# Optimization experiments

Measured on AMD Instinct MI355X. Metric: run time of the kernel, lower is better.

## Reference

```python
import jax, jax.numpy as jnp
import numpy as np

ALPHA = 0.2          # LeakyReLU negative slope
NEG_INF = -9e15      # mask fill value used by the original module


def setup_inputs() -> dict:
    key = jax.random.key(0)
    k1, k2, k3, k4 = jax.random.split(key, 4)
    N, F_in, F_out = 8192, 256, 64
    h = jax.random.normal(k1, (N, F_in), dtype=jnp.float32)
    adj = jax.random.randint(k2, (N, N), 0, 2).astype(jnp.int32)
    # xavier_uniform with gain=1.414
    gain = 1.414
    bW = gain * np.sqrt(6.0 / (F_in + F_out))
    W = jax.random.uniform(k3, (F_in, F_out), dtype=jnp.float32, minval=-bW, maxval=bW)
    ba = gain * np.sqrt(6.0 / (2 * F_out + 1))
    a = jax.random.uniform(k4, (2 * F_out, 1), dtype=jnp.float32, minval=-ba, maxval=ba)
    return {"h": h, "adj": adj, "W": W, "a": a}


def reference(h, adj, W, a):
    # Wh: [N, F_out]
    Wh = h @ W
    F_out = Wh.shape[1]
    # Decompose a_input @ a: e[i, j] = leakyrelu(Wh[j]@a[:F] + Wh[i]@a[F:])
    # (repeat gives Wh[j] in the first half, repeat_interleave gives Wh[i] in the second)
    f_src = (Wh @ a[:F_out]).reshape(-1)   # [N], coefficient of column index j
    f_dst = (Wh @ a[F_out:]).reshape(-1)   # [N], coefficient of row index i
    e = jax.nn.leaky_relu(f_dst[:, None] + f_src[None, :], negative_slope=ALPHA)  # [N, N]
    attention = jnp.where(adj > 0, e, NEG_INF)
    attention = jax.nn.softmax(attention, axis=1)
    # dropout is identity in eval mode (training=False)
    h_prime = attention @ Wh               # [N, F_out]
    return jax.nn.elu(h_prime)             # concat=True path
```

## Files before the change

kernel.cpp:

```cpp
#include <hip/hip_runtime.h>
#include <hip/hip_bf16.h>

#define GN     8192
#define FIN    256
#define FOUT   64
#define NSPLIT 8
#define JSEG   1024
#define NCH    32
#define ROWS_B 128
#define LOG2E  1.44269504f

typedef float  f32x4  __attribute__((ext_vector_type(4)));
typedef __bf16 bf16x8 __attribute__((ext_vector_type(8)));
typedef int    iv4    __attribute__((ext_vector_type(4)));

__device__ __forceinline__ unsigned short f2bf_rtne(float x) {
    unsigned int u = __float_as_uint(x);
    unsigned int r = (u + 0x7FFFu + ((u >> 16) & 1u)) >> 16;
    return (unsigned short)r;
}

__global__ __launch_bounds__(256) void k_pack(const int* __restrict__ adj,
                                              unsigned* __restrict__ bmask) {
    int wv = threadIdx.x >> 6, lane = threadIdx.x & 63;
    int w = blockIdx.x * 4 + wv;
    const int* base = adj + (size_t)w * 256 + lane * 4;
    int sh = (lane & 7) * 4;
    int hsel = lane >> 3;

    iv4 st[4];
#pragma unroll
    for (int dd = 0; dd < 4; ++dd)
        st[dd] = *(const iv4*)(base + (size_t)dd * 2097152);
#pragma unroll 4
    for (int i = 0; i < 32; ++i) {
        iv4 v = st[i & 3];
        int ni = i + 4;
        if (ni < 32)
            st[i & 3] = *(const iv4*)(base + (size_t)ni * 2097152);
        unsigned n = (unsigned)min(v[0], 1)
                   | ((unsigned)min(v[1], 1) << 1)
                   | ((unsigned)min(v[2], 1) << 2)
                   | ((unsigned)min(v[3], 1) << 3);
        unsigned x = n << sh;
        x |= __shfl_xor(x, 1);
        x |= __shfl_xor(x, 2);
        x |= __shfl_xor(x, 4);
        if ((lane & 7) == 0)
            bmask[((size_t)i * 8192 + w) * 8 + hsel] = x;
    }
}

__global__ __launch_bounds__(256) void k_wh(const float* __restrict__ h,
                                            const float* __restrict__ W,
                                            const float* __restrict__ a,
                                            float* __restrict__ fsrc,
                                            float* __restrict__ fdst,
                                            uint4* __restrict__ whfrag) {
    __shared__ float Wt[FOUT][FIN + 1];
    __shared__ float WhL[32][FOUT + 1];
    int t = threadIdx.x;
    int col = t & 63, kq4 = t >> 6;
#pragma unroll
    for (int rep = 0; rep < 16; ++rep) {
        int k0 = kq4 * 4 + rep * 16;
        float4 wv;
        wv.x = W[(k0 + 0) * FOUT + col];
        wv.y = W[(k0 + 1) * FOUT + col];
        wv.z = W[(k0 + 2) * FOUT + col];
        wv.w = W[(k0 + 3) * FOUT + col];
        *(float4*)&Wt[col][k0] = wv;
    }
    __syncthreads();
    int wave = t >> 6, lane = t & 63;
    float a1 = a[lane], a2 = a[FOUT + lane];
    int bid = blockIdx.x;
#pragma unroll
    for (int rr = 0; rr < 8; ++rr) {
        int il = wave * 8 + rr;
        int i  = bid * 32 + il;
        const float* hrow = h + (size_t)i * FIN;
        float acc = 0.f;
#pragma unroll 8
        for (int k0 = 0; k0 < FIN; k0 += 4) {
            float4 hv = *(const float4*)&hrow[k0];
            float4 wv = *(const float4*)&Wt[lane][k0];
            acc += hv.x * wv.x + hv.y * wv.y + hv.z * wv.z + hv.w * wv.w;
        }
        WhL[il][lane] = acc;
        float v1 = acc * a1, v2 = acc * a2;
#pragma unroll
        for (int off = 32; off > 0; off >>= 1) {
            v1 += __shfl_xor(v1, off);
            v2 += __shfl_xor(v2, off);
        }
        if (lane == 0) {
            fsrc[i] = fminf(v1, 30.f) * LOG2E;
            fdst[i] = fminf(v2, 30.f) * LOG2E;
        }
    }
    __syncthreads();
    int lane2 = t & 63, ct = t >> 6;
    int colc = ct * 16 + (lane2 & 15);
    int gb = lane2 >> 4;
    unsigned int pk[4];
#pragma unroll
    for (int p = 0; p < 4; ++p) {
        int jo = ((p >> 1) * 16) + gb * 4 + (p & 1) * 2;
        unsigned int lo = f2bf_rtne(WhL[jo    ][colc]);
        unsigned int hi = f2bf_rtne(WhL[jo + 1][colc]);
        pk[p] = lo | (hi << 16);
    }
    uint4 o; o.x = pk[0]; o.y = pk[1]; o.z = pk[2]; o.w = pk[3];
    whfrag[(size_t)(bid * 4 + ct) * 64 + lane2] = o;
}

__global__ __launch_bounds__(512, 1) void k_attn(const unsigned* __restrict__ bmask,
                                                 const float* __restrict__ fsrc,
                                                 const float* __restrict__ fdst,
                                                 const uint4* __restrict__ whfrag,
                                                 float* __restrict__ pacc,
                                                 float* __restrict__ pden) {
    __shared__ uint4 whL[NCH * 4 * 64];
    __shared__ float fsL[JSEG];

    int t = threadIdx.x, wv = t >> 6, lane = t & 63;
    int bid = blockIdx.x;
    int rt = bid >> 3, q = bid & (NSPLIT - 1);
    int rowbase = rt * ROWS_B;
    int r = lane & 15, g = lane >> 4;
    int row = rowbase + wv * 16 + r;

    const uint4* bm4 = (const uint4*)bmask + (size_t)row * 64 + q * 8;
    uint4 M[8];
#pragma unroll
    for (int i = 0; i < 8; ++i) M[i] = bm4[i];
    float d = fdst[row];

    {
        const uint4* src = whfrag + (size_t)q * (NCH * 4 * 64);
#pragma unroll
        for (int it = 0; it < 16; ++it) whL[it * 512 + t] = src[it * 512 + t];
        if (t < 256) *(float4*)&fsL[t * 4] = *(const float4*)&fsrc[q * JSEG + t * 4];
    }
    __syncthreads();

    f32x4 acc0 = {0.f, 0.f, 0.f, 0.f}, acc1 = acc0, acc2 = acc0, acc3 = acc0;
    float den = 0.f;

#pragma unroll
    for (int grp = 0; grp < 4; ++grp) {
#pragma unroll
        for (int chl = 0; chl < 8; ++chl) {
            int ch = grp * 8 + chl;
            uint4 Mv = M[ch >> 2];
            unsigned wb[4] = {Mv.x, Mv.y, Mv.z, Mv.w};
            unsigned Wd = wb[ch & 3];
            unsigned Wlo = Wd >> (g * 4);
            float4 s0 = *(const float4*)&fsL[ch * 32 + g * 4];
            float4 s1 = *(const float4*)&fsL[ch * 32 + 16 + g * 4];
            const uint4* bl = &whL[(ch * 4) * 64 + lane];
            uint4 b0 = bl[0], b1 = bl[64], b2 = bl[128], b3 = bl[192];
            float se[8] = {s0.x, s0.y, s0.z, s0.w, s1.x, s1.y, s1.z, s1.w};
            bf16x8 af;
            float ws = 0.f;
#pragma unroll
            for (int e = 0; e < 8; ++e) {
                float ev = d + se[e];
                float lr = fmaxf(ev, 0.2f * ev);
                float ex = __builtin_amdgcn_exp2f(lr);
                unsigned bit = (Wlo >> ((e & 3) + ((e >> 2) << 4))) & 1u;
                float wvv = bit ? ex : 0.f;
                ws += wvv;
                af[e] = (__bf16)wvv;
            }
            den += ws;
            acc0 = __builtin_amdgcn_mfma_f32_16x16x32_bf16(af, __builtin_bit_cast(bf16x8, b0), acc0, 0, 0, 0);
            acc1 = __builtin_amdgcn_mfma_f32_16x16x32_bf16(af, __builtin_bit_cast(bf16x8, b1), acc1, 0, 0, 0);
            acc2 = __builtin_amdgcn_mfma_f32_16x16x32_bf16(af, __builtin_bit_cast(bf16x8, b2), acc2, 0, 0, 0);
            acc3 = __builtin_amdgcn_mfma_f32_16x16x32_bf16(af, __builtin_bit_cast(bf16x8, b3), acc3, 0, 0, 0);
        }
    }

    den += __shfl_xor(den, 16);
    den += __shfl_xor(den, 32);

    float* po = pacc + (size_t)q * (GN * FOUT);
    int orow = rowbase + wv * 16 + g * 4;
#pragma unroll
    for (int reg = 0; reg < 4; ++reg) {
        po[(size_t)(orow + reg) * FOUT +  0 + r] = acc0[reg];
        po[(size_t)(orow + reg) * FOUT + 16 + r] = acc1[reg];
        po[(size_t)(orow + reg) * FOUT + 32 + r] = acc2[reg];
        po[(size_t)(orow + reg) * FOUT + 48 + r] = acc3[reg];
    }
    if (g == 0) pden[(size_t)q * GN + row] = den;
}

__global__ __launch_bounds__(256) void k_out(const float* __restrict__ pacc,
                                             const float* __restrict__ pden,
                                             float* __restrict__ out) {
    int idx = blockIdx.x * 256 + threadIdx.x;
    int i = idx >> 6;
    float num = 0.f, den = 0.f;
#pragma unroll
    for (int qq = 0; qq < NSPLIT; ++qq) {
        num += pacc[(size_t)qq * (GN * FOUT) + idx];
        den += pden[(size_t)qq * GN + i];
    }
    float v = (den != 0.f) ? num / den : 0.f;
    out[idx] = v > 0.f ? v : __expf(v) - 1.f;
}

extern "C" void kernel_launch(void* const* d_in, const int* in_sizes, int n_in,
                              void* d_out, int out_size, void* d_ws, size_t ws_size,
                              hipStream_t stream) {
    (void)in_sizes; (void)n_in; (void)out_size; (void)ws_size;
    const float* h   = (const float*)d_in[0];
    const int*   adj = (const int*)d_in[1];
    const float* W   = (const float*)d_in[2];
    const float* a   = (const float*)d_in[3];
    float* out = (float*)d_out;

    float* ws       = (float*)d_ws;
    float* fsrc     = ws;
    float* fdst     = fsrc + GN;
    uint4* whfrag   = (uint4*)(fdst + GN);
    float* pacc     = (float*)(whfrag + (size_t)GN / 32 * 4 * 64);
    float* pden     = pacc + (size_t)NSPLIT * GN * FOUT;
    unsigned* bmask = (unsigned*)(pden + (size_t)NSPLIT * GN);

    k_pack<<<GN / 4,                  256, 0, stream>>>(adj, bmask);
    k_wh  <<<GN / 32,                 256, 0, stream>>>(h, W, a, fsrc, fdst, whfrag);
    k_attn<<<(GN / ROWS_B) * NSPLIT,  512, 0, stream>>>(bmask, fsrc, fdst, whfrag, pacc, pden);
    k_out <<<GN * FOUT / 256,         256, 0, stream>>>(pacc, pden, out);
}
```

Measured before the change: 124.6 us.

## Transpose packed adjacency bitmask via LDS for coalesced 16-byte stores

The pack kernel no longer merges nibbles with cross-lane shuffles and then stores 4-byte words from one lane in eight. Each lane now builds its nibbles in registers, and the wave transposes them through shared memory so every lane writes one coalesced 16-byte store. The bitmask layout changes to match, so the attention kernel computes a new gather index when it loads each row's mask words. This removes the shuffles and the scattered narrow stores, but the attention-side mask loads may now be less contiguous.

```diff
diff --git a/kernel.cpp b/kernel.cpp
--- a/kernel.cpp
+++ b/kernel.cpp
@@ -21,18 +21,18 @@
 }
 
 __global__ __launch_bounds__(256) void k_pack(const int* __restrict__ adj,
-                                              unsigned* __restrict__ bmask) {
+                                              unsigned* __restrict__ bmask2) {
+    __shared__ unsigned lbuf[4][64][4];
     int wv = threadIdx.x >> 6, lane = threadIdx.x & 63;
     int w = blockIdx.x * 4 + wv;
     const int* base = adj + (size_t)w * 256 + lane * 4;
-    int sh = (lane & 7) * 4;
-    int hsel = lane >> 3;
-
+
+    unsigned pk[4] = {0u, 0u, 0u, 0u};
     iv4 st[4];
 #pragma unroll
     for (int dd = 0; dd < 4; ++dd)
         st[dd] = *(const iv4*)(base + (size_t)dd * 2097152);
-#pragma unroll 4
+#pragma unroll
     for (int i = 0; i < 32; ++i) {
         iv4 v = st[i & 3];
         int ni = i + 4;
@@ -42,13 +42,27 @@
                    | ((unsigned)min(v[1], 1) << 1)
                    | ((unsigned)min(v[2], 1) << 2)
                    | ((unsigned)min(v[3], 1) << 3);
-        unsigned x = n << sh;
-        x |= __shfl_xor(x, 1);
-        x |= __shfl_xor(x, 2);
-        x |= __shfl_xor(x, 4);
-        if ((lane & 7) == 0)
-            bmask[((size_t)i * 8192 + w) * 8 + hsel] = x;
-    }
+        pk[i >> 3] |= n << ((i & 7) * 4);
+    }
+
+    *(uint4*)&lbuf[wv][lane][0] = *(const uint4*)pk;
+    int i_own = lane >> 1;
+    int hbase = (lane & 1) * 4;
+    int rsel = i_own >> 3, nsh = (i_own & 7) * 4;
+    unsigned ow[4];
+#pragma unroll
+    for (int k = 0; k < 4; ++k) {
+        int h = hbase + k;
+        unsigned wd = 0;
+#pragma unroll
+        for (int m = 0; m < 8; ++m) {
+            unsigned nib = (lbuf[wv][8 * h + m][rsel] >> nsh) & 0xFu;
+            wd |= nib << (m * 4);
+        }
+        ow[k] = wd;
+    }
+    uint4 o; o.x = ow[0]; o.y = ow[1]; o.z = ow[2]; o.w = ow[3];
+    *(uint4*)(bmask2 + (size_t)w * 256 + lane * 4) = o;
 }
 
 __global__ __launch_bounds__(256) void k_wh(const float* __restrict__ h,
@@ -115,7 +129,7 @@
     whfrag[(size_t)(bid * 4 + ct) * 64 + lane2] = o;
 }
 
-__global__ __launch_bounds__(512, 1) void k_attn(const unsigned* __restrict__ bmask,
+__global__ __launch_bounds__(512, 1) void k_attn(const unsigned* __restrict__ bmask2,
                                                  const float* __restrict__ fsrc,
                                                  const float* __restrict__ fdst,
                                                  const uint4* __restrict__ whfrag,
@@ -131,10 +145,13 @@
     int r = lane & 15, g = lane >> 4;
     int row = rowbase + wv * 16 + r;
 
-    const uint4* bm4 = (const uint4*)bmask + (size_t)row * 64 + q * 8;
     uint4 M[8];
 #pragma unroll
-    for (int i = 0; i < 8; ++i) M[i] = bm4[i];
+    for (int i8 = 0; i8 < 8; ++i8) {
+        int p = row * 32 + q * 4 + (i8 >> 1);
+        size_t base = (size_t)(p & 8191) * 256 + (size_t)(p >> 13) * 8 + (i8 & 1) * 4;
+        M[i8] = *(const uint4*)(bmask2 + base);
+    }
     float d = fdst[row];
 
     {
```

Result: slower. 135.0 us (+8.4%).
